# Kernel optimization log

Measured on AMD Instinct MI355X. Metric: run time of the kernel, lower is better.

Reference implementation:

```python
import jax, jax.numpy as jnp
import numpy as np

B, S, HID = 4, 2048, 1024
NH, L, A = 8, 64, 64           # num_heads, linear_dim, attention_dim
NB = 128                        # time buckets
THETA = 10000.0


def _ln(x, g, b, eps=1e-5):
    m = x.mean(-1, keepdims=True)
    v = ((x - m) ** 2).mean(-1, keepdims=True)
    return (x - m) / jnp.sqrt(v + eps) * g + b


def _ln_na(x, eps=1e-5):  # F.layer_norm without affine
    m = x.mean(-1, keepdims=True)
    v = ((x - m) ** 2).mean(-1, keepdims=True)
    return (x - m) / jnp.sqrt(v + eps)


def _rope(x):
    # x: [B,H,S,A], full-dim interleaved RoPE (rope_partial_dim=0)
    inv = 1.0 / (THETA ** (jnp.arange(0, A, 2, dtype=jnp.float32) / A))
    f = jnp.arange(S, dtype=jnp.float32)[:, None] * inv[None, :]  # [S, A/2]
    cos, sin = jnp.cos(f), jnp.sin(f)
    e, o = x[..., ::2], x[..., 1::2]
    oe = e * cos - o * sin
    oo = o * cos + e * sin
    return jnp.stack([oe, oo], axis=-1).reshape(x.shape)


def setup_inputs() -> dict:
    key = jax.random.key(0)
    ks = jax.random.split(key, 12)
    x = jax.random.normal(ks[0], (B, S, HID), jnp.float32)
    interval = jnp.sort(jax.random.randint(ks[1], (B, S), 0, 1000000), axis=1).astype(jnp.int32)
    attn_mask = jnp.broadcast_to(jnp.tril(jnp.ones((S, S), bool)), (B, S, S))
    next_action_type = jax.random.randint(ks[2], (B, S), 0, 3).astype(jnp.int32)
    next_mask = jax.random.randint(ks[3], (B, S), 0, 2).astype(jnp.int32)
    uvqk = 0.02 * jax.random.normal(ks[4], (HID, 2 * L * NH + 2 * A * NH), jnp.float32)
    o_w = 0.02 * jax.random.normal(ks[5], (L * NH, HID), jnp.float32)
    pos_w = 0.02 * jax.random.normal(ks[6], (2 * S - 1,), jnp.float32)
    ts_w = 0.02 * jax.random.normal(ks[7], (NB + 1,), jnp.float32)
    act_tab = (0.02 * jax.random.normal(ks[8], (4, 32), jnp.float32)).at[0].set(0.0)
    film_w = 0.02 * jax.random.normal(ks[9], (32, 2 * HID), jnp.float32)
    return {
        'x': x, 'interval': interval, 'attn_mask': attn_mask,
        'next_action_type': next_action_type, 'next_mask': next_mask,
        'ln_g': jnp.ones(HID), 'ln_b': jnp.zeros(HID),
        'uvqk': uvqk, 'o_w': o_w, 'o_b': jnp.zeros(HID),
        'pos_w': pos_w, 'ts_w': ts_w, 'act_tab': act_tab,
        'film_ln_g': jnp.ones(32), 'film_ln_b': jnp.zeros(32),
        'film_w': film_w, 'film_b': jnp.zeros(2 * HID),
        'pr_ln_g': jnp.ones(HID), 'pr_ln_b': jnp.zeros(HID),
        'r_scale': jnp.float32(0.1), 'b_scale': jnp.float32(0.1),
    }


def reference(x, interval, attn_mask, next_action_type, next_mask,
              ln_g, ln_b, uvqk, o_w, o_b, pos_w, ts_w, act_tab,
              film_ln_g, film_ln_b, film_w, film_b, pr_ln_g, pr_ln_b,
              r_scale, b_scale):
    h = _ln(x, ln_g, ln_b)
    proj = jax.nn.silu(jnp.einsum('bsh,hd->bsd', h, uvqk))
    U = proj[..., :L * NH]
    V = proj[..., L * NH:2 * L * NH]
    Q = proj[..., 2 * L * NH:2 * L * NH + A * NH]
    K = proj[..., 2 * L * NH + A * NH:]
    U = U.reshape(B, S, NH, L).transpose(0, 2, 1, 3)
    V = V.reshape(B, S, NH, L).transpose(0, 2, 1, 3)
    Q = _rope(Q.reshape(B, S, NH, A).transpose(0, 2, 1, 3))
    K = _rope(K.reshape(B, S, NH, A).transpose(0, 2, 1, 3))
    scores = jnp.einsum('bhsa,bhta->bhst', Q, K)  # [B,H,S,S]
    # bucketized time-interval bias (indices are constants, .detach in torch)
    ts = interval.astype(jnp.float32)
    ext = jnp.concatenate([ts, ts[:, S - 1:S]], axis=1)  # [B, S+1]
    diff = ext[:, 1:, None] - ext[:, None, :-1]          # [B, S, S]
    bucket = jnp.clip((jnp.log(jnp.clip(jnp.abs(diff), 1.0, None)) / 0.301).astype(jnp.int32), 0, NB)
    scores = scores + ts_w[bucket][:, None]
    # relative position bias: bias[i,j] = pos_w[S-1 + j - i]
    rel_idx = jnp.arange(S)[None, :] - jnp.arange(S)[:, None] + (S - 1)
    scores = scores + pos_w[rel_idx][None, None]
    scores = jax.nn.silu(scores) / S
    scores = jnp.where(attn_mask[:, None], scores, 0.0)
    out = _ln_na(jnp.einsum('bhst,bhtl->bhsl', scores, V))
    u_dot = (U * out).transpose(0, 2, 1, 3).reshape(B, S, NH * L)
    outputs = x + u_dot @ o_w + o_b
    # PinRec FiLM gating
    ids = (next_action_type + 1) * (next_mask == 1)
    ae = act_tab[ids]                                    # [B,S,32]
    rb = _ln(ae, film_ln_g, film_ln_b) @ film_w + film_b
    r, b = rb[..., :HID], rb[..., HID:]
    outputs = outputs + _ln(outputs, pr_ln_g, pr_ln_b) * jnp.tanh(r) * r_scale + b * b_scale
    return outputs
```

## Files before the change

### kernel.cpp

```cpp
#include <hip/hip_runtime.h>
#include <hip/hip_bf16.h>
#include <stdint.h>

#define B_    4
#define S_    2048
#define HID_  1024
#define NH_   8
#define L_    64
#define A_    64
#define NB_   128

using bf16 = __hip_bfloat16;
typedef __bf16 bf16x8 __attribute__((ext_vector_type(8)));
typedef float  f32x4  __attribute__((ext_vector_type(4)));

__device__ __forceinline__ float bf2f(bf16 v){ return __bfloat162float(v); }
__device__ __forceinline__ bf16  f2bf(float v){ return __float2bfloat16(v); }

__device__ __forceinline__ f32x4 mfma16(bf16x8 a, bf16x8 b, f32x4 c){
  return __builtin_amdgcn_mfma_f32_16x16x32_bf16(a, b, c, 0, 0, 0);
}

__device__ __forceinline__ void gll16(const void* g, void* l){
  __builtin_amdgcn_global_load_lds(
      (const __attribute__((address_space(1))) unsigned int*)g,
      (__attribute__((address_space(3))) unsigned int*)l, 16, 0, 0);
}

__global__ __launch_bounds__(256) void k_tcast(const float* __restrict__ src,
                                               bf16* __restrict__ dst, int R, int C){
  __shared__ float t[32][33];
  int c0 = blockIdx.x*32, r0 = blockIdx.y*32;
  int tx = threadIdx.x & 31, ty = threadIdx.x >> 5;
#pragma unroll
  for (int j=0;j<4;j++) t[ty+j*8][tx] = src[(size_t)(r0+ty+j*8)*C + c0+tx];
  __syncthreads();
#pragma unroll
  for (int j=0;j<4;j++) dst[(size_t)(c0+ty+j*8)*R + r0+tx] = f2bf(t[tx][ty+j*8]);
}

__global__ void k_rb4(const float* __restrict__ act_tab, const float* __restrict__ fg,
                      const float* __restrict__ fb, const float* __restrict__ fw,
                      const float* __restrict__ fbias, float* __restrict__ rb4){
  __shared__ float lnae[4][32];
  __shared__ float mv[4][2];
  int tid = threadIdx.x;
  if (tid < 128) lnae[tid>>5][tid&31] = act_tab[tid];
  __syncthreads();
  if (tid < 4){
    float s=0.f, q=0.f;
#pragma unroll
    for (int i=0;i<32;i++){ float a=lnae[tid][i]; s+=a; q+=a*a; }
    float mean = s*(1.f/32.f);
    mv[tid][0] = mean;
    mv[tid][1] = rsqrtf(q*(1.f/32.f) - mean*mean + 1e-5f);
  }
  __syncthreads();
  if (tid < 128){
    int id=tid>>5, i=tid&31;
    lnae[id][i] = (lnae[id][i]-mv[id][0])*mv[id][1]*fg[i] + fb[i];
  }
  __syncthreads();
  for (int idx=tid; idx<4*2048; idx+=256){
    int id = idx>>11, j = idx&2047;
    float acc = fbias[j];
#pragma unroll
    for (int i=0;i<32;i++) acc += lnae[id][i]*fw[i*2048+j];
    rb4[idx] = acc;
  }
}

__global__ __launch_bounds__(256) void k_ln_x(const float* __restrict__ x,
      const float* __restrict__ g, const float* __restrict__ bta, bf16* __restrict__ h){
  int row = blockIdx.x; int tid = threadIdx.x;
  const float* xr = x + (size_t)row*HID_;
  float v[4]; float sum=0.f, sq=0.f;
#pragma unroll
  for (int i=0;i<4;i++){ v[i]=xr[tid + i*256]; sum+=v[i]; sq+=v[i]*v[i]; }
#pragma unroll
  for (int o=1;o<64;o<<=1){ sum+=__shfl_xor(sum,o,64); sq+=__shfl_xor(sq,o,64); }
  __shared__ float red[2][4];
  int wid=tid>>6, lane=tid&63;
  if(lane==0){ red[0][wid]=sum; red[1][wid]=sq; }
  __syncthreads();
  sum = red[0][0]+red[0][1]+red[0][2]+red[0][3];
  sq  = red[1][0]+red[1][1]+red[1][2]+red[1][3];
  float mean = sum*(1.f/HID_);
  float rstd = rsqrtf(sq*(1.f/HID_)-mean*mean + 1e-5f);
#pragma unroll
  for (int i=0;i<4;i++){
    int c = tid+i*256;
    h[(size_t)row*HID_ + c] = f2bf((v[i]-mean)*rstd*g[c] + bta[c]);
  }
}

__global__ __launch_bounds__(256) void k_gemm_uvqk(const bf16* __restrict__ hb,
        const bf16* __restrict__ wT, bf16* __restrict__ proj){
  __shared__ __align__(16) ushort shA[128*32];
  __shared__ __align__(16) ushort shB[128*32];
  const int K = 1024;
  int bx = blockIdx.x;
  int tm = bx & 63, tn = bx >> 6;
  int brow = tm*128, bcol = tn*128;
  int tid = threadIdx.x;
  int wid = tid>>6, lane = tid&63, lr = lane&15, lg = lane>>4;
  int wm = wid>>1, wn = wid&1;
  f32x4 acc[4][4] = {};
  for (int k0=0; k0<K; k0+=32){
    __syncthreads();
#pragma unroll
    for (int i=0;i<2;i++){
      int c = tid + i*256;
      int row = c>>2, kp = (c&3)*8;
      gll16(&hb[(size_t)(brow+row)*K + k0+kp], &shA[c*8]);
      gll16(&wT[(size_t)(bcol+row)*K + k0+kp], &shB[c*8]);
    }
    __syncthreads();
    bf16x8 a[4], b[4];
#pragma unroll
    for (int m=0;m<4;m++) a[m] = *(const bf16x8*)&shA[(wm*64+m*16+lr)*32 + lg*8];
#pragma unroll
    for (int n=0;n<4;n++) b[n] = *(const bf16x8*)&shB[(wn*64+n*16+lr)*32 + lg*8];
#pragma unroll
    for (int m=0;m<4;m++)
#pragma unroll
      for (int n=0;n<4;n++)
        acc[m][n] = mfma16(a[m], b[n], acc[m][n]);
  }
#pragma unroll
  for (int m=0;m<4;m++)
#pragma unroll
    for (int n=0;n<4;n++)
#pragma unroll
      for (int r=0;r<4;r++){
        int row = brow + wm*64+m*16+lg*4+r;
        int col = bcol + wn*64+n*16+lr;
        float v = acc[m][n][r];
        proj[(size_t)row*2048 + col] = f2bf(v / (1.f + __expf(-v)));
      }
}

__global__ __launch_bounds__(256) void k_rope(bf16* __restrict__ proj){
  int row = blockIdx.x;
  int s = row & (S_-1);
  int t = threadIdx.x;
  int h = t >> 5, p = t & 31;
  const float L2_10000 = 13.287712379549449f;
  float inv = exp2f(-(float)p * (L2_10000/32.f));
  float f = (float)s * inv;
  float sn, c; sincosf(f, &sn, &c);
  size_t base = (size_t)row*2048;
  int cq = 1024 + h*64 + 2*p;
  float qe = bf2f(proj[base+cq]), qo = bf2f(proj[base+cq+1]);
  proj[base+cq]   = f2bf(qe*c - qo*sn);
  proj[base+cq+1] = f2bf(qo*c + qe*sn);
  int ck = 1536 + h*64 + 2*p;
  float ke = bf2f(proj[base+ck]), ko = bf2f(proj[base+ck+1]);
  proj[base+ck]   = f2bf(ke*c - ko*sn);
  proj[base+ck+1] = f2bf(ko*c + ke*sn);
}

__global__ __launch_bounds__(256) void k_vtrans(const bf16* __restrict__ proj, bf16* __restrict__ Vt){
  __shared__ __align__(16) ushort lds[32][520];
  int bx = blockIdx.x; int b = bx>>6; int s0 = (bx&63)*32;
  int tid = threadIdx.x;
#pragma unroll
  for (int i=0;i<8;i++){
    int c = tid + i*256;
    int sl = c>>6, e8 = (c&63)*8;
    *(uint4*)&lds[sl][e8] = *(const uint4*)&proj[((size_t)(b*S_+s0+sl))*2048 + 512 + e8];
  }
  __syncthreads();
#pragma unroll
  for (int q=0;q<2;q++){
    int hl = tid + q*256;
    ushort v[32];
#pragma unroll
    for (int j=0;j<32;j++) v[j] = lds[j][hl];
#pragma unroll
    for (int w=0;w<4;w++)
      *(uint4*)&Vt[((size_t)b*512 + hl)*S_ + s0 + w*8] = *(uint4*)&v[w*8];
  }
}

__global__ __launch_bounds__(256) void k_bias_sw(const int* __restrict__ interval,
      const float* __restrict__ ts_w, const float* __restrict__ pos_w,
      bf16* __restrict__ bsw){
  __shared__ int   itvL[2048];
  __shared__ float posL[2080];
  __shared__ float tsL[132];
  int bx = blockIdx.x;
  int b  = bx & 3;
  int st = 63 - (bx >> 2);
  int tid = threadIdx.x, wid = tid>>6, lane = tid&63, lr = lane&15, lg = lane>>4;
  const int* itv = interval + b*S_;
  for (int i=tid;i<2048;i+=256) itvL[i]=itv[i];
  int pbase = 2016 - st*32;
  int plen  = st*32 + 63;
  for (int i=tid;i<plen;i+=256) posL[i] = pos_w[pbase + i];
  if (tid<129) tsL[tid]=ts_w[tid];
  __syncthreads();
  size_t tbase = (size_t)b*2080 + (size_t)(st*(st+1)/2);
  for (int tt = wid; tt <= st; tt += 4){
    ushort ov[16];
#pragma unroll
    for (int m=0;m<2;m++)
#pragma unroll
      for (int n=0;n<2;n++)
#pragma unroll
        for (int r=0;r<4;r++){
          int sl = m*16 + lg*4 + r;
          int sg = st*32 + sl;
          int tg = tt*32 + n*16 + lr;
          float val;
          if (tg <= sg){
            int sp = sg+1; if (sp>2047) sp=2047;
            float d = fmaxf(fabsf((float)(itvL[sp]-itvL[tg])),1.f);
            int bk = (int)(__log2f(d)*2.3027481f);
            bk = bk<0?0:(bk>NB_?NB_:bk);
            val = tsL[bk] + posL[tg - sl + 31];
          } else val = -10000.f;
          ov[m*8+n*4+r] = __bfloat16_as_ushort(f2bf(val));
        }
    bf16* dst = bsw + ((tbase + tt)*64 + lane)*16;
    *(uint4*)dst     = *(uint4*)&ov[0];
    *(uint4*)(dst+8) = *(uint4*)&ov[8];
  }
}

__global__ __launch_bounds__(256, 4) void k_attn(const bf16* __restrict__ proj,
     const bf16* __restrict__ Vt, const bf16* __restrict__ bsw,
     bf16* __restrict__ u_dot){
  __shared__ __align__(16) char smem[16640];
  bf16  (*Plds)[32][36]  = (bf16 (*)[32][36])smem;
  float (*redbuf)[16][65] = (float(*)[16][65])smem;
  int bx = blockIdx.x;
  int st = bx >> 5;
  int h  = (bx >> 2) & 7;
  int b  = bx & 3;
  int s0 = st*32;
  int tid = threadIdx.x, wid = tid>>6, lane = tid&63, lr = lane&15, lg = lane>>4;
  size_t rowb = (size_t)b * S_;

  bf16x8 aq[2][2];
#pragma unroll
  for (int m=0;m<2;m++)
#pragma unroll
    for (int ks=0;ks<2;ks++)
      aq[m][ks] = *(const bf16x8*)&proj[(rowb + s0 + m*16 + lr)*2048 + 1024 + h*64 + ks*32 + lg*8];

  size_t tbase = (size_t)b*2080 + (size_t)(st*(st+1)/2);
  f32x4 acc[2][4] = {};
  int nT = st + 1;
  for (int tt = wid; tt < nT; tt += 4){
    int t0 = tt*32;
    bf16x8 kb[2][2];
#pragma unroll
    for (int n=0;n<2;n++)
#pragma unroll
      for (int ks=0;ks<2;ks++)
        kb[n][ks] = *(const bf16x8*)&proj[(rowb + t0 + n*16 + lr)*2048 + 1536 + h*64 + ks*32 + lg*8];
    const bf16* bp = bsw + ((tbase + tt)*64 + lane)*16;
    bf16x8 bb0 = *(const bf16x8*)bp;
    bf16x8 bb1 = *(const bf16x8*)(bp+8);
    bf16x8 bv[4];
#pragma unroll
    for (int n=0;n<4;n++)
      bv[n] = *(const bf16x8*)&Vt[((size_t)b*512 + h*64 + n*16+lr)*S_ + t0 + lg*8];
    f32x4 sacc[2][2] = {};
#pragma unroll
    for (int m=0;m<2;m++)
#pragma unroll
      for (int n=0;n<2;n++)
#pragma unroll
        for (int ks=0;ks<2;ks++)
          sacc[m][n] = mfma16(aq[m][ks], kb[n][ks], sacc[m][n]);
#pragma unroll
    for (int m=0;m<2;m++)
#pragma unroll
      for (int n=0;n<2;n++)
#pragma unroll
        for (int r2=0;r2<4;r2++){
          float bvv = bf2f(m ? (bf16)bb1[n*4+r2] : (bf16)bb0[n*4+r2]);
          float v  = sacc[m][n][r2] + bvv;
          float p  = v * __builtin_amdgcn_rcpf(1.f + __expf(-v));
          Plds[wid][m*16 + lg*4 + r2][n*16 + lr] = f2bf(p);
        }
    bf16x8 pa[2];
#pragma unroll
    for (int m=0;m<2;m++) pa[m] = *(const bf16x8*)&Plds[wid][m*16+lr][lg*8];
#pragma unroll
    for (int n=0;n<4;n++)
#pragma unroll
      for (int m=0;m<2;m++)
        acc[m][n] = mfma16(pa[m], bv[n], acc[m][n]);
  }

#pragma unroll
  for (int m=0;m<2;m++){
    __syncthreads();
#pragma unroll
    for (int n=0;n<4;n++)
#pragma unroll
      for (int r2=0;r2<4;r2++)
        redbuf[wid][lg*4+r2][n*16+lr] = acc[m][n][r2];
    __syncthreads();
#pragma unroll
    for (int q=0;q<4;q++){
      int rr = wid*4 + q;
      float v = (redbuf[0][rr][lane] + redbuf[1][rr][lane]
               + redbuf[2][rr][lane] + redbuf[3][rr][lane]) * (1.f/(float)S_);
      float sum = v, sq = v*v;
#pragma unroll
      for (int o=1;o<64;o<<=1){ sum += __shfl_xor(sum,o,64); sq += __shfl_xor(sq,o,64); }
      float mean = sum*(1.f/64.f);
      float rstd = rsqrtf(sq*(1.f/64.f) - mean*mean + 1e-5f);
      int sg = s0 + m*16 + rr;
      float u = bf2f(proj[(rowb+sg)*2048 + h*64 + lane]);
      u_dot[(rowb+sg)*512 + h*64 + lane] = f2bf((v-mean)*rstd*u);
    }
  }
}

__global__ __launch_bounds__(256) void k_gemm_out(const bf16* __restrict__ ud,
        const bf16* __restrict__ wT, const float* __restrict__ x,
        const float* __restrict__ ob, float* __restrict__ out){
  __shared__ __align__(16) ushort shA[128*32];
  __shared__ __align__(16) ushort shB[128*32];
  const int K = 512;
  int bx = blockIdx.x;
  int tm = bx & 63, tn = bx >> 6;
  int brow = tm*128, bcol = tn*128;
  int tid = threadIdx.x;
  int wid = tid>>6, lane = tid&63, lr = lane&15, lg = lane>>4;
  int wm = wid>>1, wn = wid&1;
  f32x4 acc[4][4] = {};
  for (int k0=0; k0<K; k0+=32){
    __syncthreads();
#pragma unroll
    for (int i=0;i<2;i++){
      int c = tid + i*256;
      int row = c>>2, kp = (c&3)*8;
      gll16(&ud[(size_t)(brow+row)*K + k0+kp], &shA[c*8]);
      gll16(&wT[(size_t)(bcol+row)*K + k0+kp], &shB[c*8]);
    }
    __syncthreads();
    bf16x8 a[4], b[4];
#pragma unroll
    for (int m=0;m<4;m++) a[m] = *(const bf16x8*)&shA[(wm*64+m*16+lr)*32 + lg*8];
#pragma unroll
    for (int n=0;n<4;n++) b[n] = *(const bf16x8*)&shB[(wn*64+n*16+lr)*32 + lg*8];
#pragma unroll
    for (int m=0;m<4;m++)
#pragma unroll
      for (int n=0;n<4;n++)
        acc[m][n] = mfma16(a[m], b[n], acc[m][n]);
  }
#pragma unroll
  for (int m=0;m<4;m++)
#pragma unroll
    for (int n=0;n<4;n++)
#pragma unroll
      for (int r=0;r<4;r++){
        int row = brow + wm*64+m*16+lg*4+r;
        int col = bcol + wn*64+n*16+lr;
        out[(size_t)row*HID_ + col] = acc[m][n][r] + x[(size_t)row*HID_ + col] + ob[col];
      }
}

__global__ __launch_bounds__(256) void k_film(float* __restrict__ out,
   const float* __restrict__ rb4, const int* __restrict__ nat, const int* __restrict__ nm,
   const float* __restrict__ prg, const float* __restrict__ prb,
   const float* __restrict__ rsp, const float* __restrict__ bsp){
  int row = blockIdx.x; int tid = threadIdx.x;
  float* orow = out + (size_t)row*HID_;
  int id = (nat[row] + 1) * (nm[row]==1 ? 1 : 0);
  float rs = rsp[0], bs = bsp[0];
  float v[4]; float sum=0.f, sq=0.f;
#pragma unroll
  for (int i=0;i<4;i++){ v[i]=orow[tid+i*256]; sum+=v[i]; sq+=v[i]*v[i]; }
#pragma unroll
  for (int o=1;o<64;o<<=1){ sum+=__shfl_xor(sum,o,64); sq+=__shfl_xor(sq,o,64); }
  __shared__ float red[2][4];
  int wid=tid>>6, lane=tid&63;
  if(lane==0){ red[0][wid]=sum; red[1][wid]=sq; }
  __syncthreads();
  sum = red[0][0]+red[0][1]+red[0][2]+red[0][3];
  sq  = red[1][0]+red[1][1]+red[1][2]+red[1][3];
  float mean = sum*(1.f/HID_);
  float rstd = rsqrtf(sq*(1.f/HID_)-mean*mean + 1e-5f);
#pragma unroll
  for (int i=0;i<4;i++){
    int c = tid+i*256;
    float ln = (v[i]-mean)*rstd*prg[c]+prb[c];
    float r  = rb4[id*2048 + c];
    float b2 = rb4[id*2048 + 1024 + c];
    orow[c] = v[i] + ln*tanhf(r)*rs + b2*bs;
  }
}

extern "C" void kernel_launch(void* const* d_in, const int* in_sizes, int n_in,
                              void* d_out, int out_size, void* d_ws, size_t ws_size,
                              hipStream_t stream){
  const float* x        = (const float*)d_in[0];
  const int*   interval = (const int*)d_in[1];
  const int*   nat      = (const int*)d_in[3];
  const int*   nm       = (const int*)d_in[4];
  const float* ln_g     = (const float*)d_in[5];
  const float* ln_b     = (const float*)d_in[6];
  const float* uvqk     = (const float*)d_in[7];
  const float* o_w      = (const float*)d_in[8];
  const float* o_b      = (const float*)d_in[9];
  const float* pos_w    = (const float*)d_in[10];
  const float* ts_w     = (const float*)d_in[11];
  const float* act_tab  = (const float*)d_in[12];
  const float* film_g   = (const float*)d_in[13];
  const float* film_bt  = (const float*)d_in[14];
  const float* film_w   = (const float*)d_in[15];
  const float* film_b   = (const float*)d_in[16];
  const float* pr_g     = (const float*)d_in[17];
  const float* pr_b     = (const float*)d_in[18];
  const float* r_scale  = (const float*)d_in[19];
  const float* b_scale  = (const float*)d_in[20];
  float* out = (float*)d_out;

  char* ws = (char*)d_ws;
  bf16*  uvqkT = (bf16*)(ws);
  bf16*  o_wT  = (bf16*)(ws + (4u<<20));
  float* rb4   = (float*)(ws + (5u<<20));
  bf16*  hb    = (bf16*)(ws + (6u<<20));
  bf16*  Vt    = (bf16*)(ws + (6u<<20));
  bf16*  ud    = (bf16*)(ws + (14u<<20));
  bf16*  proj  = (bf16*)(ws + (22u<<20));
  bf16*  bsw   = (bf16*)(ws + (54u<<20));

  k_tcast<<<dim3(2048/32, 1024/32), 256, 0, stream>>>(uvqk, uvqkT, 1024, 2048);
  k_tcast<<<dim3(1024/32,  512/32), 256, 0, stream>>>(o_w,  o_wT,   512, 1024);
  k_rb4<<<1, 256, 0, stream>>>(act_tab, film_g, film_bt, film_w, film_b, rb4);
  k_bias_sw<<<256, 256, 0, stream>>>(interval, ts_w, pos_w, bsw);
  k_ln_x<<<B_*S_, 256, 0, stream>>>(x, ln_g, ln_b, hb);
  k_gemm_uvqk<<<64*16, 256, 0, stream>>>(hb, uvqkT, proj);
  k_rope<<<B_*S_, 256, 0, stream>>>(proj);
  k_vtrans<<<B_*64, 256, 0, stream>>>(proj, Vt);
  k_attn<<<64*32, 256, 0, stream>>>(proj, Vt, bsw, ud);
  k_gemm_out<<<64*8, 256, 0, stream>>>(ud, o_wT, x, o_b, out);
  k_film<<<B_*S_, 256, 0, stream>>>(out, rb4, nat, nm, pr_g, pr_b, r_scale, b_scale);
}
```

Before: 247.3 us.

## Fuse RoPE into projection GEMM epilogue and reorder causal attention tiles

RoPE on Q and K is now applied inside the UVQK GEMM epilogue, using a lane shuffle to fetch the paired even/odd element. This removes the separate k_rope kernel and its extra read-modify-write pass over proj. Attention blocks are launched longest-first by reversing the query-tile index, which should even out the load from the causal mask. The occupancy hint for k_attn is raised from 4 to 6, which may force register spills. The fast __sinf/__cosf are less accurate than sincosf for large angles (s up to 2047), so precision may drop.

```diff
diff --git a/kernel.cpp b/kernel.cpp
--- a/kernel.cpp
+++ b/kernel.cpp
@@ -127,6 +127,8 @@
       for (int n=0;n<4;n++)
         acc[m][n] = mfma16(a[m], b[n], acc[m][n]);
   }
+  const float RL = 13.287712379549449f/32.f;
+  bool isQK = (tn >= 8);
 #pragma unroll
   for (int m=0;m<4;m++)
 #pragma unroll
@@ -136,28 +138,17 @@
         int row = brow + wm*64+m*16+lg*4+r;
         int col = bcol + wn*64+n*16+lr;
         float v = acc[m][n][r];
-        proj[(size_t)row*2048 + col] = f2bf(v / (1.f + __expf(-v)));
+        v = v / (1.f + __expf(-v));
+        if (isQK){
+          float vp = __shfl_xor(v, 1, 64);
+          int   s  = row & (S_-1);
+          int   p  = (n*16+lr) >> 1;
+          float f  = (float)s * exp2f(-(float)p * RL);
+          float sn = __sinf(f), cs = __cosf(f);
+          v = (lr & 1) ? (v*cs + vp*sn) : (v*cs - vp*sn);
+        }
+        proj[(size_t)row*2048 + col] = f2bf(v);
       }
-}
-
-__global__ __launch_bounds__(256) void k_rope(bf16* __restrict__ proj){
-  int row = blockIdx.x;
-  int s = row & (S_-1);
-  int t = threadIdx.x;
-  int h = t >> 5, p = t & 31;
-  const float L2_10000 = 13.287712379549449f;
-  float inv = exp2f(-(float)p * (L2_10000/32.f));
-  float f = (float)s * inv;
-  float sn, c; sincosf(f, &sn, &c);
-  size_t base = (size_t)row*2048;
-  int cq = 1024 + h*64 + 2*p;
-  float qe = bf2f(proj[base+cq]), qo = bf2f(proj[base+cq+1]);
-  proj[base+cq]   = f2bf(qe*c - qo*sn);
-  proj[base+cq+1] = f2bf(qo*c + qe*sn);
-  int ck = 1536 + h*64 + 2*p;
-  float ke = bf2f(proj[base+ck]), ko = bf2f(proj[base+ck+1]);
-  proj[base+ck]   = f2bf(ke*c - ko*sn);
-  proj[base+ck+1] = f2bf(ko*c + ke*sn);
 }
 
 __global__ __launch_bounds__(256) void k_vtrans(const bf16* __restrict__ proj, bf16* __restrict__ Vt){
@@ -228,14 +219,14 @@
   }
 }
 
-__global__ __launch_bounds__(256, 4) void k_attn(const bf16* __restrict__ proj,
+__global__ __launch_bounds__(256, 6) void k_attn(const bf16* __restrict__ proj,
      const bf16* __restrict__ Vt, const bf16* __restrict__ bsw,
      bf16* __restrict__ u_dot){
   __shared__ __align__(16) char smem[16640];
   bf16  (*Plds)[32][36]  = (bf16 (*)[32][36])smem;
   float (*redbuf)[16][65] = (float(*)[16][65])smem;
   int bx = blockIdx.x;
-  int st = bx >> 5;
+  int st = 63 - (bx >> 5);
   int h  = (bx >> 2) & 7;
   int b  = bx & 3;
   int s0 = st*32;
@@ -440,7 +431,6 @@
   k_bias_sw<<<256, 256, 0, stream>>>(interval, ts_w, pos_w, bsw);
   k_ln_x<<<B_*S_, 256, 0, stream>>>(x, ln_g, ln_b, hb);
   k_gemm_uvqk<<<64*16, 256, 0, stream>>>(hb, uvqkT, proj);
-  k_rope<<<B_*S_, 256, 0, stream>>>(proj);
   k_vtrans<<<B_*64, 256, 0, stream>>>(proj, Vt);
   k_attn<<<64*32, 256, 0, stream>>>(proj, Vt, bsw, ud);
   k_gemm_out<<<64*8, 256, 0, stream>>>(ud, o_wT, x, o_b, out);
```

Measured after the change: 253.9 us. 2.7% more time.
